# Performance work log

Measured on AMD Instinct MI355X. Metric: run time of the kernel, lower is better.

## Reference

```python
import jax, jax.numpy as jnp
import numpy as np

B, T, NINP, NHID = 64, 256, 256, 512
NTOK0, NTOK1 = 2048, 512


def _lstm_cell(x, h, c, Wih, bih, Whh, bhh):
    # PyTorch LSTMCell gate order: i, f, g, o
    g = x @ Wih.T + bih + h @ Whh.T + bhh
    i, f, gg, o = jnp.split(g, 4, axis=-1)
    c_new = jax.nn.sigmoid(f) * c + jax.nn.sigmoid(i) * jnp.tanh(gg)
    h_new = jax.nn.sigmoid(o) * jnp.tanh(c_new)
    return h_new, c_new


def setup_inputs() -> dict:
    key = jax.random.key(0)
    ks = jax.random.split(key, 16)
    ir = 0.1  # initrange from init_weights
    d = {
        "input0": jax.random.randint(ks[0], (B, T), 0, NTOK0),
        "input1": jax.random.randint(ks[1], (B, T), 0, NTOK1),
        "h_low0": jnp.zeros((B, NHID), jnp.float32),
        "c_low0": jnp.zeros((B, NHID), jnp.float32),
        "h_high0": jnp.zeros((B, NHID), jnp.float32),
        "c_high0": jnp.zeros((B, NHID), jnp.float32),
        "measure_token_idx": 5,
        "emb0": jax.random.uniform(ks[2], (NTOK0, NINP), jnp.float32, -ir, ir),
        "emb1": jax.random.uniform(ks[3], (NTOK1, NINP), jnp.float32, -ir, ir),
        # low cell: input size = ninp*2 + nhid = 1024
        "Wih_low": jax.random.normal(ks[4], (4 * NHID, 2 * NINP + NHID), jnp.float32) * 0.02,
        "bih_low": jnp.zeros((4 * NHID,), jnp.float32),
        "Whh_low": jax.random.normal(ks[5], (4 * NHID, NHID), jnp.float32) * 0.02,
        "bhh_low": jnp.zeros((4 * NHID,), jnp.float32),
        # high cell: input size = nhid
        "Wih_high": jax.random.normal(ks[6], (4 * NHID, NHID), jnp.float32) * 0.02,
        "bih_high": jnp.zeros((4 * NHID,), jnp.float32),
        "Whh_high": jax.random.normal(ks[7], (4 * NHID, NHID), jnp.float32) * 0.02,
        "bhh_high": jnp.zeros((4 * NHID,), jnp.float32),
        "Wdec0": jax.random.uniform(ks[8], (NTOK0, NHID), jnp.float32, -ir, ir),
        "bdec0": jnp.zeros((NTOK0,), jnp.float32),
        "Wdec1": jax.random.uniform(ks[9], (NTOK1, NHID), jnp.float32, -ir, ir),
        "bdec1": jnp.zeros((NTOK1,), jnp.float32),
    }
    return d


def reference(input0, input1, h_low0, c_low0, h_high0, c_high0, measure_token_idx,
              emb0, emb1, Wih_low, bih_low, Whh_low, bhh_low,
              Wih_high, bih_high, Whh_high, bhh_high,
              Wdec0, bdec0, Wdec1, bdec1):
    # Embedding lookups for both channels, concatenated (dropout = identity in eval)
    embs = jnp.concatenate([emb0[input0], emb1[input1]], axis=-1)  # [B,T,2*ninp]
    xs = jnp.swapaxes(embs, 0, 1)                                   # [T,B,2*ninp]
    mask = (input0 == measure_token_idx).astype(embs.dtype)[..., None]  # [B,T,1]
    ms = jnp.swapaxes(mask, 0, 1)                                   # [T,B,1]

    def step(carry, xm):
        h_l, c_l, h_h, c_h = carry
        x_t, m_t = xm
        inp = jnp.concatenate([x_t, h_h], axis=-1)  # [B, 2*ninp+nhid]
        h_l, c_l = _lstm_cell(inp, h_l, c_l, Wih_low, bih_low, Whh_low, bhh_low)
        h_tmp, c_tmp = _lstm_cell(h_l, h_h, c_h, Wih_high, bih_high, Whh_high, bhh_high)
        h_h = m_t * h_tmp + (1.0 - m_t) * h_h  # gated state update at measure boundaries
        c_h = m_t * c_tmp + (1.0 - m_t) * c_h
        return (h_l, c_l, h_h, c_h), h_l

    (h_l, c_l, h_h, c_h), outs = jax.lax.scan(step, (h_low0, c_low0, h_high0, c_high0), (xs, ms))
    output = jnp.swapaxes(outs, 0, 1)  # [B,T,nhid]
    dec0 = output @ Wdec0.T + bdec0    # [B,T,ntok0]
    dec1 = output @ Wdec1.T + bdec1    # [B,T,ntok1]
    return dec0, dec1, h_l, c_l, h_h, c_h
```

## Files before the change

kernel.cpp:

```cpp
#include <hip/hip_runtime.h>
#include <hip/hip_bf16.h>

#define T_ 256
#define B_ 64
#define NWG 32

typedef __attribute__((ext_vector_type(8))) short bf16x8;
typedef __attribute__((ext_vector_type(4))) float f32x4;

__device__ __forceinline__ float bf2f(unsigned short u){
  unsigned int i = ((unsigned int)u) << 16;
  float f; __builtin_memcpy(&f, &i, 4); return f;
}
__device__ __forceinline__ unsigned short f2bf(float f){
  __hip_bfloat16 h = __float2bfloat16(f);
  unsigned short u; __builtin_memcpy(&u, &h, 2); return u;
}
__device__ __forceinline__ float sigm(float x){ return 1.0f/(1.0f + expf(-x)); }

__device__ __forceinline__ bf16x8 ld_h8(const unsigned short* p){
  union { unsigned long long q[2]; bf16x8 v; } u;
  u.q[0] = __hip_atomic_load((const unsigned long long*)p,       __ATOMIC_RELAXED, __HIP_MEMORY_SCOPE_AGENT);
  u.q[1] = __hip_atomic_load((const unsigned long long*)(p + 4), __ATOMIC_RELAXED, __HIP_MEMORY_SCOPE_AGENT);
  return u.v;
}
__device__ __forceinline__ void st_h4(unsigned short* p, unsigned short a, unsigned short b,
                                      unsigned short c, unsigned short d){
  unsigned long long v = (unsigned long long)a | ((unsigned long long)b<<16)
                       | ((unsigned long long)c<<32) | ((unsigned long long)d<<48);
  __hip_atomic_store((unsigned long long*)p, v, __ATOMIC_RELAXED, __HIP_MEMORY_SCOPE_AGENT);
}
__device__ __forceinline__ unsigned long long ld_h4(const unsigned short* p){
  return __hip_atomic_load((const unsigned long long*)p, __ATOMIC_RELAXED, __HIP_MEMORY_SCOPE_AGENT);
}

__global__ void k_prep(const int* __restrict__ in0, const int* __restrict__ in1,
                       const int* __restrict__ mtok,
                       const float* __restrict__ emb0, const float* __restrict__ emb1,
                       const float* __restrict__ Wih_low, const float* __restrict__ Whh_low_f,
                       const float* __restrict__ Wih_high_f, const float* __restrict__ Whh_high_f,
                       const float* __restrict__ Wdec0_f, const float* __restrict__ Wdec1_f,
                       unsigned short* __restrict__ W0, unsigned short* __restrict__ Wlh,
                       unsigned short* __restrict__ Whhl, unsigned short* __restrict__ Wihh,
                       unsigned short* __restrict__ Whhh, unsigned short* __restrict__ Wd0,
                       unsigned short* __restrict__ Wd1, unsigned short* __restrict__ E,
                       float* __restrict__ mask, unsigned* __restrict__ stepflag,
                       unsigned* __restrict__ bar)
{
  int gid = blockIdx.x*blockDim.x + threadIdx.x;
  int gsz = gridDim.x*blockDim.x;
  for (int i=gid; i<2048*512; i+=gsz){
    int r = i>>9, c = i&511;
    W0[i]   = f2bf(Wih_low[(size_t)r*1024 + c]);
    Wlh[i]  = f2bf(Wih_low[(size_t)r*1024 + 512 + c]);
    Whhl[i] = f2bf(Whh_low_f[i]);
    Wihh[i] = f2bf(Wih_high_f[i]);
    Whhh[i] = f2bf(Whh_high_f[i]);
    Wd0[i]  = f2bf(Wdec0_f[i]);
  }
  for (int i=gid; i<512*512; i+=gsz) Wd1[i] = f2bf(Wdec1_f[i]);
  int mt = mtok[0];
  for (int i=gid; i<T_*B_*512; i+=gsz){
    int m = i>>9, k = i&511;
    int t = m>>6, b = m&63;
    float v;
    if (k < 256) v = emb0[(size_t)in0[b*T_+t]*256 + k];
    else         v = emb1[(size_t)in1[b*T_+t]*256 + (k-256)];
    E[i] = f2bf(v);
  }
  for (int i=gid; i<T_*B_; i+=gsz){
    int t = i>>6, b = i&63;
    mask[i] = (in0[b*T_+t] == mt) ? 1.0f : 0.0f;
  }
  for (int i=gid; i<T_; i+=gsz){
    unsigned f = 0;
    for (int b=0;b<B_;b++) f |= (in0[b*T_+i] == mt) ? 1u : 0u;
    stepflag[i] = f;
  }
  if (gid == 0){ bar[0] = 0; bar[32] = 0; }
}

__launch_bounds__(256)
__global__ void k_gemm(const unsigned short* __restrict__ A,
                       const unsigned short* __restrict__ W,
                       const float* __restrict__ bias1, const float* __restrict__ bias2,
                       unsigned short* __restrict__ out16, float* __restrict__ out32,
                       int N, int mode)
{
  __shared__ unsigned short As[128*40];
  __shared__ unsigned short Bs[128*40];
  const int tid = threadIdx.x;
  const int m0 = blockIdx.x*128, n0 = blockIdx.y*128;
  const int wid = tid>>6, lane = tid&63;
  const int wm = (wid>>1)*64, wn = (wid&1)*64;
  const int lr = lane&15, lk = lane>>4;
  f32x4 acc[4][4] = {};
  for (int k0=0; k0<512; k0+=32){
    __syncthreads();
    #pragma unroll
    for (int i=0;i<2;i++){
      int eb = tid + 256*i;
      int row = eb>>2, kb = eb&3;
      *(bf16x8*)&As[row*40 + kb*8] = *(const bf16x8*)&A[(size_t)(m0+row)*512 + k0 + kb*8];
      *(bf16x8*)&Bs[row*40 + kb*8] = *(const bf16x8*)&W[(size_t)(n0+row)*512 + k0 + kb*8];
    }
    __syncthreads();
    bf16x8 af[4], bff[4];
    #pragma unroll
    for (int i=0;i<4;i++){
      af[i]  = *(const bf16x8*)&As[(wm + i*16 + lr)*40 + lk*8];
      bff[i] = *(const bf16x8*)&Bs[(wn + i*16 + lr)*40 + lk*8];
    }
    #pragma unroll
    for (int mi=0;mi<4;mi++)
      #pragma unroll
      for (int ni=0;ni<4;ni++)
        acc[mi][ni] = __builtin_amdgcn_mfma_f32_16x16x32_bf16(af[mi], bff[ni], acc[mi][ni], 0,0,0);
  }
  #pragma unroll
  for (int mi=0;mi<4;mi++){
    #pragma unroll
    for (int ni=0;ni<4;ni++){
      int n = n0 + wn + ni*16 + lr;
      float bb = bias1 ? bias1[n] : 0.0f;
      if (bias2) bb += bias2[n];
      #pragma unroll
      for (int r=0;r<4;r++){
        int m = m0 + wm + mi*16 + lk*4 + r;
        float v = acc[mi][ni][r] + bb;
        if (mode == 0){
          out16[(size_t)m*N + n] = f2bf(v);
        } else {
          int t = m>>6, b = m&63;
          out32[((size_t)b*T_ + t)*N + n] = v;
        }
      }
    }
  }
}

__device__ __forceinline__ void gbarrier(unsigned* bar, unsigned gen){
  __syncthreads();
  if (threadIdx.x == 0){
    unsigned old = __hip_atomic_fetch_add(&bar[0], 1u, __ATOMIC_RELAXED, __HIP_MEMORY_SCOPE_AGENT);
    if (old == gen*NWG + (NWG-1)){
      __hip_atomic_store(&bar[32], gen+1u, __ATOMIC_RELAXED, __HIP_MEMORY_SCOPE_AGENT);
    } else {
      while (__hip_atomic_load(&bar[32], __ATOMIC_RELAXED, __HIP_MEMORY_SCOPE_AGENT) < gen+1u)
        __builtin_amdgcn_s_sleep(1);
    }
  }
  __builtin_amdgcn_sched_barrier(0);
  __syncthreads();
  __builtin_amdgcn_sched_barrier(0);
}

__device__ __forceinline__ void compute_hht(const unsigned short* __restrict__ hh,
                                            const unsigned short* __restrict__ Wlh,
                                            float* hht, int d0, int mb, int lr, int lk)
{
  bf16x8 av[16];
  #pragma unroll
  for (int ks=0;ks<16;ks++)
    av[ks] = ld_h8(&hh[(mb+lr)*512 + ks*32 + lk*8]);
  f32x4 a[4] = {};
  #pragma unroll
  for (int ks=0;ks<16;ks++){
    #pragma unroll
    for (int g=0; g<4; g++){
      bf16x8 bg = *(const bf16x8*)&Wlh[(size_t)(g*512 + d0 + lr)*512 + ks*32 + lk*8];
      a[g] = __builtin_amdgcn_mfma_f32_16x16x32_bf16(av[ks], bg, a[g], 0,0,0);
    }
  }
  #pragma unroll
  for (int g=0; g<4; g++)
    #pragma unroll
    for (int r=0;r<4;r++){
      int b = mb + lk*4 + r;
      hht[b*68 + g*16 + lr] = a[g][r];
    }
}

__launch_bounds__(256)
__global__ void k_recur(const float* __restrict__ h_low0, const float* __restrict__ c_low0,
                        const float* __restrict__ h_high0, const float* __restrict__ c_high0,
                        const float* __restrict__ bih_high, const float* __restrict__ bhh_high,
                        const unsigned short* __restrict__ xW,
                        const unsigned short* __restrict__ Whhl,
                        const unsigned short* __restrict__ Wlh,
                        const unsigned short* __restrict__ Wihh,
                        const unsigned short* __restrict__ Whhh,
                        const float* __restrict__ mask, const unsigned* __restrict__ stepflag,
                        unsigned short* __restrict__ hl_buf, unsigned short* __restrict__ hh_buf,
                        unsigned short* __restrict__ hseq, unsigned* bar,
                        float* __restrict__ outS)
{
  __shared__ unsigned short Ws[64*520];
  __shared__ float hht[64*68];
  __shared__ float gb[64*68];
  __shared__ float cl[64*16];
  __shared__ float ch[64*16];
  const int tid = threadIdx.x;
  const int j = blockIdx.x;
  const int d0 = j*16;
  const int wid = tid>>6, lane = tid&63;
  const int lr = lane&15, lk = lane>>4;
  const int mb = wid*16;
  const int eb = tid>>2;
  const int ep = (tid&3)*4;

  for (int i=tid; i<64*64; i+=256){
    int n = i>>6, cb = i&63;
    int grow = (n>>4)*512 + d0 + (n&15);
    *(bf16x8*)&Ws[n*520 + cb*8] = *(const bf16x8*)&Whhl[(size_t)grow*512 + cb*8];
  }
  for (int i=tid; i<1024; i+=256){
    int b=i>>4, dd=i&15;
    cl[i] = c_low0[b*512 + d0 + dd];
    ch[i] = c_high0[b*512 + d0 + dd];
  }
  {
    int gi = eb*512 + d0 + ep;
    st_h4(&hl_buf[gi], f2bf(h_low0[gi]), f2bf(h_low0[gi+1]), f2bf(h_low0[gi+2]), f2bf(h_low0[gi+3]));
    st_h4(&hh_buf[gi], f2bf(h_high0[gi]), f2bf(h_high0[gi+1]), f2bf(h_high0[gi+2]), f2bf(h_high0[gi+3]));
  }
  unsigned long long uxi, uxf, uxg, uxo;
  {
    size_t xr = ((size_t)0*64 + eb)*2048 + d0 + ep;
    uxi = *(const unsigned long long*)&xW[xr];
    uxf = *(const unsigned long long*)&xW[xr + 512];
    uxg = *(const unsigned long long*)&xW[xr + 1024];
    uxo = *(const unsigned long long*)&xW[xr + 1536];
  }
  unsigned gen = 0;
  gbarrier(bar, gen); gen++;
  compute_hht(hh_buf, Wlh, hht, d0, mb, lr, lk);
  __syncthreads();

  int hs = 0;
  for (int t=0; t<T_; t++){
    const int rl = t&1, wl = rl^1;
    const unsigned short* hlr = hl_buf + rl*32768;
    bf16x8 av[16];
    #pragma unroll
    for (int ks=0;ks<16;ks++)
      av[ks] = ld_h8(&hlr[(mb+lr)*512 + ks*32 + lk*8]);
    f32x4 a[4] = {};
    #pragma unroll
    for (int ks=0;ks<16;ks++){
      #pragma unroll
      for (int g=0; g<4; g++){
        bf16x8 bg = *(const bf16x8*)&Ws[(g*16+lr)*520 + ks*32 + lk*8];
        a[g] = __builtin_amdgcn_mfma_f32_16x16x32_bf16(av[ks], bg, a[g], 0,0,0);
      }
    }
    #pragma unroll
    for (int g=0; g<4; g++)
      #pragma unroll
      for (int r=0;r<4;r++){
        int b = mb + lk*4 + r;
        gb[b*68 + g*16 + lr] = a[g][r] + hht[b*68 + g*16 + lr];
      }
    __syncthreads();
    {
      const int b = eb;
      unsigned short hb[4];
      #pragma unroll
      for (int q=0;q<4;q++){
        int dd = ep + q;
        float g_i = gb[b*68 + dd]      + bf2f((unsigned short)(uxi >> (16*q)));
        float g_f = gb[b*68 + 16 + dd] + bf2f((unsigned short)(uxf >> (16*q)));
        float g_g = gb[b*68 + 32 + dd] + bf2f((unsigned short)(uxg >> (16*q)));
        float g_o = gb[b*68 + 48 + dd] + bf2f((unsigned short)(uxo >> (16*q)));
        float c = sigm(g_f)*cl[b*16+dd] + sigm(g_i)*tanhf(g_g);
        float h = sigm(g_o)*tanhf(c);
        cl[b*16+dd] = c;
        hb[q] = f2bf(h);
      }
      st_h4(&hl_buf[wl*32768 + b*512 + d0 + ep], hb[0], hb[1], hb[2], hb[3]);
      unsigned long long hp = (unsigned long long)hb[0] | ((unsigned long long)hb[1]<<16)
                            | ((unsigned long long)hb[2]<<32) | ((unsigned long long)hb[3]<<48);
      *(unsigned long long*)&hseq[((size_t)t*64 + b)*512 + d0 + ep] = hp;
    }
    if (t+1 < T_){
      size_t xr = ((size_t)(t+1)*64 + eb)*2048 + d0 + ep;
      uxi = *(const unsigned long long*)&xW[xr];
      uxf = *(const unsigned long long*)&xW[xr + 512];
      uxg = *(const unsigned long long*)&xW[xr + 1024];
      uxo = *(const unsigned long long*)&xW[xr + 1536];
    }
    gbarrier(bar, gen); gen++;
    if (stepflag[t]){
      const unsigned short* hln = hl_buf + wl*32768;
      const unsigned short* hhr = hh_buf + hs*32768;
      bf16x8 avl[16], avh[16];
      #pragma unroll
      for (int ks=0;ks<16;ks++){
        avl[ks] = ld_h8(&hln[(mb+lr)*512 + ks*32 + lk*8]);
        avh[ks] = ld_h8(&hhr[(mb+lr)*512 + ks*32 + lk*8]);
      }
      f32x4 hacc[4] = {};
      #pragma unroll
      for (int ks=0;ks<16;ks++){
        #pragma unroll
        for (int g=0; g<4; g++){
          size_t grw = (size_t)(g*512 + d0 + lr)*512 + ks*32 + lk*8;
          bf16x8 bi = *(const bf16x8*)&Wihh[grw];
          bf16x8 bh = *(const bf16x8*)&Whhh[grw];
          hacc[g] = __builtin_amdgcn_mfma_f32_16x16x32_bf16(avl[ks], bi, hacc[g], 0,0,0);
          hacc[g] = __builtin_amdgcn_mfma_f32_16x16x32_bf16(avh[ks], bh, hacc[g], 0,0,0);
        }
      }
      #pragma unroll
      for (int g=0; g<4; g++)
        #pragma unroll
        for (int r=0;r<4;r++){
          int b = mb + lk*4 + r;
          gb[b*68 + g*16 + lr] = hacc[g][r];
        }
      __syncthreads();
      {
        const int b = eb;
        float m = mask[t*64 + b];
        unsigned long long hold4 = ld_h4(&hh_buf[hs*32768 + b*512 + d0 + ep]);
        unsigned short hn[4];
        #pragma unroll
        for (int q=0;q<4;q++){
          int dd = ep + q; int d = d0 + dd;
          float g_i = gb[b*68+dd]      + bih_high[d]      + bhh_high[d];
          float g_f = gb[b*68+16+dd]   + bih_high[512+d]  + bhh_high[512+d];
          float g_g = gb[b*68+32+dd]   + bih_high[1024+d] + bhh_high[1024+d];
          float g_o = gb[b*68+48+dd]   + bih_high[1536+d] + bhh_high[1536+d];
          float ct = sigm(g_f)*ch[b*16+dd] + sigm(g_i)*tanhf(g_g);
          float ht = sigm(g_o)*tanhf(ct);
          float hold = bf2f((unsigned short)(hold4 >> (16*q)));
          hn[q] = f2bf(m*ht + (1.0f-m)*hold);
          ch[b*16+dd] = m*ct + (1.0f-m)*ch[b*16+dd];
        }
        st_h4(&hh_buf[(hs^1)*32768 + b*512 + d0 + ep], hn[0], hn[1], hn[2], hn[3]);
      }
      gbarrier(bar, gen); gen++;
      hs ^= 1;
      compute_hht(hh_buf + hs*32768, Wlh, hht, d0, mb, lr, lk);
      __syncthreads();
    }
  }
  {
    int gi = eb*512 + d0 + ep;
    unsigned long long hl4 = ld_h4(&hl_buf[gi]);
    unsigned long long hh4 = ld_h4(&hh_buf[hs*32768 + gi]);
    #pragma unroll
    for (int q=0;q<4;q++){
      outS[gi+q]           = bf2f((unsigned short)(hl4 >> (16*q)));
      outS[32768 + gi + q] = cl[eb*16 + ep + q];
      outS[65536 + gi + q] = bf2f((unsigned short)(hh4 >> (16*q)));
      outS[98304 + gi + q] = ch[eb*16 + ep + q];
    }
  }
}

extern "C" void kernel_launch(void* const* d_in, const int* in_sizes, int n_in,
                              void* d_out, int out_size, void* d_ws, size_t ws_size,
                              hipStream_t stream)
{
  const int*   in0    = (const int*)  d_in[0];
  const int*   in1    = (const int*)  d_in[1];
  const float* hl0    = (const float*)d_in[2];
  const float* cl0    = (const float*)d_in[3];
  const float* hh0    = (const float*)d_in[4];
  const float* ch0    = (const float*)d_in[5];
  const int*   mtok   = (const int*)  d_in[6];
  const float* emb0   = (const float*)d_in[7];
  const float* emb1   = (const float*)d_in[8];
  const float* Wihl_f = (const float*)d_in[9];
  const float* bihl   = (const float*)d_in[10];
  const float* Whhl_f = (const float*)d_in[11];
  const float* bhhl   = (const float*)d_in[12];
  const float* Wihh_f = (const float*)d_in[13];
  const float* bihh   = (const float*)d_in[14];
  const float* Whhh_f = (const float*)d_in[15];
  const float* bhhh   = (const float*)d_in[16];
  const float* Wd0_f  = (const float*)d_in[17];
  const float* bd0    = (const float*)d_in[18];
  const float* Wd1_f  = (const float*)d_in[19];
  const float* bd1    = (const float*)d_in[20];

  float* dout = (float*)d_out;
  unsigned short* xW = (unsigned short*)dout;
  unsigned short* E  = (unsigned short*)(dout + 33554432);

  char* ws = (char*)d_ws;
  unsigned short* hseq = (unsigned short*)(ws + 0);
  unsigned short* W0   = (unsigned short*)(ws + 16777216);
  unsigned short* Wlh  = (unsigned short*)(ws + 18874368);
  unsigned short* Whhl = (unsigned short*)(ws + 20971520);
  unsigned short* Wihh = (unsigned short*)(ws + 23068672);
  unsigned short* Whhh = (unsigned short*)(ws + 25165824);
  unsigned short* Wd0  = (unsigned short*)(ws + 27262976);
  unsigned short* Wd1  = (unsigned short*)(ws + 29360128);
  unsigned short* hlb  = (unsigned short*)(ws + 29884416);
  unsigned short* hhb  = (unsigned short*)(ws + 30015488);
  float*          mask = (float*)    (ws + 30146560);
  unsigned*       sflg = (unsigned*) (ws + 30212096);
  unsigned*       bar  = (unsigned*) (ws + 30213120);

  k_prep<<<2048, 256, 0, stream>>>(in0,in1,mtok,emb0,emb1,Wihl_f,Whhl_f,Wihh_f,Whhh_f,Wd0_f,Wd1_f,
                                   W0,Wlh,Whhl,Wihh,Whhh,Wd0,Wd1,E,mask,sflg,bar);
  dim3 g1(128,16);
  k_gemm<<<g1, 256, 0, stream>>>(E, W0, bihl, bhhl, xW, nullptr, 2048, 0);
  k_recur<<<NWG, 256, 0, stream>>>(hl0,cl0,hh0,ch0,bihh,bhhh,xW,Whhl,Wlh,Wihh,Whhh,
                                   mask,sflg,hlb,hhb,hseq,bar,dout + 41943040);
  k_gemm<<<g1, 256, 0, stream>>>(hseq, Wd0, bd0, nullptr, nullptr, dout, 2048, 1);
  dim3 g2(128,4);
  k_gemm<<<g2, 256, 0, stream>>>(hseq, Wd1, bd1, nullptr, nullptr, dout + 33554432, 512, 1);
}
```

Before: 2.398 ms.

## Replace atomic counter grid barrier with per-workgroup flag arrive/wait split

Replaces the single fetch-add counter barrier with per-workgroup generation flags, each padded onto its own cache line. Every workgroup stores its own flag, and one wavefront polls all 32 flags, combining the results with a ballot. The arrive is split from the wait so the next step's xW prefetch loads are issued between them, overlapping that global load latency with the barrier. This removes contention on the single atomic counter and the serialized last-arriver release store. The cost is that every waiter now polls 32 flags.

```diff
diff --git a/kernel.cpp b/kernel.cpp
--- a/kernel.cpp
+++ b/kernel.cpp
@@ -77,7 +77,7 @@
     for (int b=0;b<B_;b++) f |= (in0[b*T_+i] == mt) ? 1u : 0u;
     stepflag[i] = f;
   }
-  if (gid == 0){ bar[0] = 0; bar[32] = 0; }
+  for (int i=gid; i<1024; i+=gsz) bar[i] = 0;
 }
 
 __launch_bounds__(256)
@@ -139,15 +139,20 @@
   }
 }
 
-__device__ __forceinline__ void gbarrier(unsigned* bar, unsigned gen){
+__device__ __forceinline__ void g_arrive(unsigned* flags, int j, unsigned gen){
   __syncthreads();
-  if (threadIdx.x == 0){
-    unsigned old = __hip_atomic_fetch_add(&bar[0], 1u, __ATOMIC_RELAXED, __HIP_MEMORY_SCOPE_AGENT);
-    if (old == gen*NWG + (NWG-1)){
-      __hip_atomic_store(&bar[32], gen+1u, __ATOMIC_RELAXED, __HIP_MEMORY_SCOPE_AGENT);
-    } else {
-      while (__hip_atomic_load(&bar[32], __ATOMIC_RELAXED, __HIP_MEMORY_SCOPE_AGENT) < gen+1u)
-        __builtin_amdgcn_s_sleep(1);
+  if (threadIdx.x == 0)
+    __hip_atomic_store(&flags[j*32], gen+1u, __ATOMIC_RELAXED, __HIP_MEMORY_SCOPE_AGENT);
+  __builtin_amdgcn_sched_barrier(0);
+}
+__device__ __forceinline__ void g_wait(const unsigned* flags, unsigned gen){
+  if (threadIdx.x < 64){
+    int l = threadIdx.x;
+    for(;;){
+      unsigned v = (l < NWG) ? __hip_atomic_load(&flags[l*32], __ATOMIC_RELAXED, __HIP_MEMORY_SCOPE_AGENT)
+                             : 0xffffffffu;
+      if (__ballot(v >= gen+1u) == ~0ull) break;
+      __builtin_amdgcn_s_sleep(1);
     }
   }
   __builtin_amdgcn_sched_barrier(0);
@@ -224,6 +229,8 @@
     st_h4(&hl_buf[gi], f2bf(h_low0[gi]), f2bf(h_low0[gi+1]), f2bf(h_low0[gi+2]), f2bf(h_low0[gi+3]));
     st_h4(&hh_buf[gi], f2bf(h_high0[gi]), f2bf(h_high0[gi+1]), f2bf(h_high0[gi+2]), f2bf(h_high0[gi+3]));
   }
+  unsigned gen = 0;
+  g_arrive(bar, j, gen);
   unsigned long long uxi, uxf, uxg, uxo;
   {
     size_t xr = ((size_t)0*64 + eb)*2048 + d0 + ep;
@@ -232,8 +239,8 @@
     uxg = *(const unsigned long long*)&xW[xr + 1024];
     uxo = *(const unsigned long long*)&xW[xr + 1536];
   }
-  unsigned gen = 0;
-  gbarrier(bar, gen); gen++;
+  __builtin_amdgcn_sched_barrier(0);
+  g_wait(bar, gen); gen++;
   compute_hht(hh_buf, Wlh, hht, d0, mb, lr, lk);
   __syncthreads();
 
@@ -282,6 +289,7 @@
                             | ((unsigned long long)hb[2]<<32) | ((unsigned long long)hb[3]<<48);
       *(unsigned long long*)&hseq[((size_t)t*64 + b)*512 + d0 + ep] = hp;
     }
+    g_arrive(bar, j, gen);
     if (t+1 < T_){
       size_t xr = ((size_t)(t+1)*64 + eb)*2048 + d0 + ep;
       uxi = *(const unsigned long long*)&xW[xr];
@@ -289,7 +297,8 @@
       uxg = *(const unsigned long long*)&xW[xr + 1024];
       uxo = *(const unsigned long long*)&xW[xr + 1536];
     }
-    gbarrier(bar, gen); gen++;
+    __builtin_amdgcn_sched_barrier(0);
+    g_wait(bar, gen); gen++;
     if (stepflag[t]){
       const unsigned short* hln = hl_buf + wl*32768;
       const unsigned short* hhr = hh_buf + hs*32768;
@@ -339,7 +348,8 @@
         }
         st_h4(&hh_buf[(hs^1)*32768 + b*512 + d0 + ep], hn[0], hn[1], hn[2], hn[3]);
       }
-      gbarrier(bar, gen); gen++;
+      g_arrive(bar, j, gen);
+      g_wait(bar, gen); gen++;
       hs ^= 1;
       compute_hht(hh_buf + hs*32768, Wlh, hht, d0, mb, lr, lk);
       __syncthreads();
```

Measured after the change: 2.242 ms. -6.5%, faster.

## Replace global workgroup barrier with per-wave flag sync and fast activations

Applied to the files above, without the earlier changes.

Replaces the atomic-counter grid barrier, which was wrapped in __syncthreads, with per-wavefront arrival flags. Each wave now polls only the 32 flags of the same wave index across workgroups, so the intra-block __syncthreads calls are removed, assuming each wave only reads rows it wrote. The next step's xW loads are issued earlier so they overlap the MFMA work. sigmoid and tanh switch to __expf-based approximations, which trades some accuracy for lower latency on the serial critical path.

```diff
diff --git a/kernel.cpp b/kernel.cpp
--- a/kernel.cpp
+++ b/kernel.cpp
@@ -16,7 +16,8 @@
   __hip_bfloat16 h = __float2bfloat16(f);
   unsigned short u; __builtin_memcpy(&u, &h, 2); return u;
 }
-__device__ __forceinline__ float sigm(float x){ return 1.0f/(1.0f + expf(-x)); }
+__device__ __forceinline__ float fsigm(float x){ return 1.0f/(1.0f + __expf(-x)); }
+__device__ __forceinline__ float ftanh(float x){ return 1.0f - 2.0f/(__expf(2.0f*x) + 1.0f); }
 
 __device__ __forceinline__ bf16x8 ld_h8(const unsigned short* p){
   union { unsigned long long q[2]; bf16x8 v; } u;
@@ -24,10 +25,7 @@
   u.q[1] = __hip_atomic_load((const unsigned long long*)(p + 4), __ATOMIC_RELAXED, __HIP_MEMORY_SCOPE_AGENT);
   return u.v;
 }
-__device__ __forceinline__ void st_h4(unsigned short* p, unsigned short a, unsigned short b,
-                                      unsigned short c, unsigned short d){
-  unsigned long long v = (unsigned long long)a | ((unsigned long long)b<<16)
-                       | ((unsigned long long)c<<32) | ((unsigned long long)d<<48);
+__device__ __forceinline__ void st_h4(unsigned short* p, unsigned long long v){
   __hip_atomic_store((unsigned long long*)p, v, __ATOMIC_RELAXED, __HIP_MEMORY_SCOPE_AGENT);
 }
 __device__ __forceinline__ unsigned long long ld_h4(const unsigned short* p){
@@ -77,7 +75,7 @@
     for (int b=0;b<B_;b++) f |= (in0[b*T_+i] == mt) ? 1u : 0u;
     stepflag[i] = f;
   }
-  if (gid == 0){ bar[0] = 0; bar[32] = 0; }
+  for (int i=gid; i<1024; i+=gsz) bar[i] = 0;
 }
 
 __launch_bounds__(256)
@@ -139,19 +137,19 @@
   }
 }
 
-__device__ __forceinline__ void gbarrier(unsigned* bar, unsigned gen){
-  __syncthreads();
-  if (threadIdx.x == 0){
-    unsigned old = __hip_atomic_fetch_add(&bar[0], 1u, __ATOMIC_RELAXED, __HIP_MEMORY_SCOPE_AGENT);
-    if (old == gen*NWG + (NWG-1)){
-      __hip_atomic_store(&bar[32], gen+1u, __ATOMIC_RELAXED, __HIP_MEMORY_SCOPE_AGENT);
-    } else {
-      while (__hip_atomic_load(&bar[32], __ATOMIC_RELAXED, __HIP_MEMORY_SCOPE_AGENT) < gen+1u)
-        __builtin_amdgcn_s_sleep(1);
-    }
-  }
+__device__ __forceinline__ void w_arrive(unsigned* flags, int w, int j, unsigned gen){
+  asm volatile("s_waitcnt vmcnt(0)" ::: "memory");
+  if ((threadIdx.x & 63) == 0)
+    __hip_atomic_store(&flags[(w*NWG + j)*8], gen+1u, __ATOMIC_RELAXED, __HIP_MEMORY_SCOPE_AGENT);
   __builtin_amdgcn_sched_barrier(0);
-  __syncthreads();
+}
+__device__ __forceinline__ void w_wait(const unsigned* flags, int w, unsigned gen){
+  const unsigned* fp = &flags[(w*NWG + (threadIdx.x & (NWG-1)))*8];
+  for(;;){
+    unsigned v = __hip_atomic_load(fp, __ATOMIC_RELAXED, __HIP_MEMORY_SCOPE_AGENT);
+    if (__ballot(v >= gen+1u) == ~0ull) break;
+    __builtin_amdgcn_s_sleep(1);
+  }
   __builtin_amdgcn_sched_barrier(0);
 }
 
@@ -221,21 +219,26 @@
   }
   {
     int gi = eb*512 + d0 + ep;
-    st_h4(&hl_buf[gi], f2bf(h_low0[gi]), f2bf(h_low0[gi+1]), f2bf(h_low0[gi+2]), f2bf(h_low0[gi+3]));
-    st_h4(&hh_buf[gi], f2bf(h_high0[gi]), f2bf(h_high0[gi+1]), f2bf(h_high0[gi+2]), f2bf(h_high0[gi+3]));
-  }
-  unsigned long long uxi, uxf, uxg, uxo;
+    unsigned long long l0 = (unsigned long long)f2bf(h_low0[gi])        | ((unsigned long long)f2bf(h_low0[gi+1])<<16)
+                          | ((unsigned long long)f2bf(h_low0[gi+2])<<32)| ((unsigned long long)f2bf(h_low0[gi+3])<<48);
+    unsigned long long h0 = (unsigned long long)f2bf(h_high0[gi])        | ((unsigned long long)f2bf(h_high0[gi+1])<<16)
+                          | ((unsigned long long)f2bf(h_high0[gi+2])<<32)| ((unsigned long long)f2bf(h_high0[gi+3])<<48);
+    st_h4(&hl_buf[gi], l0);
+    st_h4(&hh_buf[gi], h0);
+  }
+  __syncthreads();
+  unsigned gen = 0;
+  w_arrive(bar, wid, j, gen);
+  w_wait(bar, wid, gen); gen++;
+  unsigned long long cxi, cxf, cxg, cxo, nxi, nxf, nxg, nxo;
   {
-    size_t xr = ((size_t)0*64 + eb)*2048 + d0 + ep;
-    uxi = *(const unsigned long long*)&xW[xr];
-    uxf = *(const unsigned long long*)&xW[xr + 512];
-    uxg = *(const unsigned long long*)&xW[xr + 1024];
-    uxo = *(const unsigned long long*)&xW[xr + 1536];
-  }
-  unsigned gen = 0;
-  gbarrier(bar, gen); gen++;
+    size_t xr = (size_t)eb*2048 + d0 + ep;
+    cxi = *(const unsigned long long*)&xW[xr];
+    cxf = *(const unsigned long long*)&xW[xr + 512];
+    cxg = *(const unsigned long long*)&xW[xr + 1024];
+    cxo = *(const unsigned long long*)&xW[xr + 1536];
+  }
   compute_hht(hh_buf, Wlh, hht, d0, mb, lr, lk);
-  __syncthreads();
 
   int hs = 0;
   for (int t=0; t<T_; t++){
@@ -245,6 +248,13 @@
     #pragma unroll
     for (int ks=0;ks<16;ks++)
       av[ks] = ld_h8(&hlr[(mb+lr)*512 + ks*32 + lk*8]);
+    if (t+1 < T_){
+      size_t xr = ((size_t)(t+1)*64 + eb)*2048 + d0 + ep;
+      nxi = *(const unsigned long long*)&xW[xr];
+      nxf = *(const unsigned long long*)&xW[xr + 512];
+      nxg = *(const unsigned long long*)&xW[xr + 1024];
+      nxo = *(const unsigned long long*)&xW[xr + 1536];
+    }
     f32x4 a[4] = {};
     #pragma unroll
     for (int ks=0;ks<16;ks++){
@@ -261,35 +271,30 @@
         int b = mb + lk*4 + r;
         gb[b*68 + g*16 + lr] = a[g][r] + hht[b*68 + g*16 + lr];
       }
-    __syncthreads();
+    unsigned long long hp;
     {
       const int b = eb;
       unsigned short hb[4];
       #pragma unroll
       for (int q=0;q<4;q++){
         int dd = ep + q;
-        float g_i = gb[b*68 + dd]      + bf2f((unsigned short)(uxi >> (16*q)));
-        float g_f = gb[b*68 + 16 + dd] + bf2f((unsigned short)(uxf >> (16*q)));
-        float g_g = gb[b*68 + 32 + dd] + bf2f((unsigned short)(uxg >> (16*q)));
-        float g_o = gb[b*68 + 48 + dd] + bf2f((unsigned short)(uxo >> (16*q)));
-        float c = sigm(g_f)*cl[b*16+dd] + sigm(g_i)*tanhf(g_g);
-        float h = sigm(g_o)*tanhf(c);
+        float g_i = gb[b*68 + dd]      + bf2f((unsigned short)(cxi >> (16*q)));
+        float g_f = gb[b*68 + 16 + dd] + bf2f((unsigned short)(cxf >> (16*q)));
+        float g_g = gb[b*68 + 32 + dd] + bf2f((unsigned short)(cxg >> (16*q)));
+        float g_o = gb[b*68 + 48 + dd] + bf2f((unsigned short)(cxo >> (16*q)));
+        float c = fsigm(g_f)*cl[b*16+dd] + fsigm(g_i)*ftanh(g_g);
+        float h = fsigm(g_o)*ftanh(c);
         cl[b*16+dd] = c;
         hb[q] = f2bf(h);
       }
-      st_h4(&hl_buf[wl*32768 + b*512 + d0 + ep], hb[0], hb[1], hb[2], hb[3]);
-      unsigned long long hp = (unsigned long long)hb[0] | ((unsigned long long)hb[1]<<16)
-                            | ((unsigned long long)hb[2]<<32) | ((unsigned long long)hb[3]<<48);
+      hp = (unsigned long long)hb[0] | ((unsigned long long)hb[1]<<16)
+         | ((unsigned long long)hb[2]<<32) | ((unsigned long long)hb[3]<<48);
+      st_h4(&hl_buf[wl*32768 + b*512 + d0 + ep], hp);
       *(unsigned long long*)&hseq[((size_t)t*64 + b)*512 + d0 + ep] = hp;
     }
-    if (t+1 < T_){
-      size_t xr = ((size_t)(t+1)*64 + eb)*2048 + d0 + ep;
-      uxi = *(const unsigned long long*)&xW[xr];
-      uxf = *(const unsigned long long*)&xW[xr + 512];
-      uxg = *(const unsigned long long*)&xW[xr + 1024];
-      uxo = *(const unsigned long long*)&xW[xr + 1536];
-    }
-    gbarrier(bar, gen); gen++;
+    w_arrive(bar, wid, j, gen);
+    w_wait(bar, wid, gen); gen++;
+    cxi = nxi; cxf = nxf; cxg = nxg; cxo = nxo;
     if (stepflag[t]){
       const unsigned short* hln = hl_buf + wl*32768;
       const unsigned short* hhr = hh_buf + hs*32768;
@@ -318,7 +323,6 @@
           int b = mb + lk*4 + r;
           gb[b*68 + g*16 + lr] = hacc[g][r];
         }
-      __syncthreads();
       {
         const int b = eb;
         float m = mask[t*64 + b];
@@ -331,18 +335,20 @@
           float g_f = gb[b*68+16+dd]   + bih_high[512+d]  + bhh_high[512+d];
           float g_g = gb[b*68+32+dd]   + bih_high[1024+d] + bhh_high[1024+d];
           float g_o = gb[b*68+48+dd]   + bih_high[1536+d] + bhh_high[1536+d];
-          float ct = sigm(g_f)*ch[b*16+dd] + sigm(g_i)*tanhf(g_g);
-          float ht = sigm(g_o)*tanhf(ct);
+          float ct = fsigm(g_f)*ch[b*16+dd] + fsigm(g_i)*ftanh(g_g);
+          float ht = fsigm(g_o)*ftanh(ct);
           float hold = bf2f((unsigned short)(hold4 >> (16*q)));
           hn[q] = f2bf(m*ht + (1.0f-m)*hold);
           ch[b*16+dd] = m*ct + (1.0f-m)*ch[b*16+dd];
         }
-        st_h4(&hh_buf[(hs^1)*32768 + b*512 + d0 + ep], hn[0], hn[1], hn[2], hn[3]);
-      }
-      gbarrier(bar, gen); gen++;
+        unsigned long long hq = (unsigned long long)hn[0] | ((unsigned long long)hn[1]<<16)
+                              | ((unsigned long long)hn[2]<<32) | ((unsigned long long)hn[3]<<48);
+        st_h4(&hh_buf[(hs^1)*32768 + eb*512 + d0 + ep], hq);
+      }
+      w_arrive(bar, wid, j, gen);
+      w_wait(bar, wid, gen); gen++;
       hs ^= 1;
       compute_hht(hh_buf + hs*32768, Wlh, hht, d0, mb, lr, lk);
-      __syncthreads();
     }
   }
   {
```

After: 2.443 ms. About the same (+1.9%).
